# Kernel tuning notes

Hardware: AMD Instinct MI355X
Metric: run time of the kernel (lower is better)

Reference implementation:

```python
import jax, jax.numpy as jnp
import numpy as np

N_NODES = 100000
N_EDGES = 1600000
N_GRAPHS = 256
D = 128      # d_graph
H = 256      # hidden
VOCAB = 30000
OUT = 2


def setup_inputs() -> dict:
    key = jax.random.key(0)
    ks = jax.random.split(key, 24)
    def lin(k, fin, fout):
        s = 1.0 / np.sqrt(fin)
        kw, kb = jax.random.split(k)
        return (jax.random.uniform(kw, (fin, fout), jnp.float32, -s, s),
                jax.random.uniform(kb, (fout,), jnp.float32, -s, s))
    inp = {
        'feat': jax.random.randint(ks[0], (N_NODES,), 0, VOCAB),
        'src': jax.random.randint(ks[1], (N_EDGES,), 0, N_NODES),
        'dst': jax.random.randint(ks[2], (N_EDGES,), 0, N_NODES),
        'graph_id': jnp.sort(jax.random.randint(ks[3], (N_NODES,), 0, N_GRAPHS)),
        'emb': jax.random.normal(ks[4], (VOCAB, D), jnp.float32),
    }
    # SAGEConv layer 0/1: fc_self + fc_neigh + bias (mean aggregator)
    inp['ws0'], _ = lin(ks[5], D, D)
    inp['wn0'], inp['b0'] = lin(ks[6], D, D)
    inp['ws1'], _ = lin(ks[7], D, D)
    inp['wn1'], inp['b1'] = lin(ks[8], D, D)
    inp['e1_w'], inp['e1_b'] = lin(ks[9], D, H)
    inp['e2_w'], inp['e2_b'] = lin(ks[10], H, H)
    inp['e3_w'], inp['e3_b'] = lin(ks[11], H, H)
    inp['e4_w'], inp['e4_b'] = lin(ks[12], H, H)
    inp['pred_w'], inp['pred_b'] = lin(ks[13], H, OUT)
    return inp


def _sage_mean(h, src, dst, ws, wn, b):
    # gather src features, mean-scatter to dst (DGL SAGEConv 'mean')
    msg = jnp.take(h, src, axis=0)                       # [E, D]
    agg = jax.ops.segment_sum(msg, dst, num_segments=N_NODES)
    deg = jax.ops.segment_sum(jnp.ones((src.shape[0],), h.dtype), dst,
                              num_segments=N_NODES)
    h_neigh = agg / jnp.maximum(deg, 1.0)[:, None]
    return h @ ws + h_neigh @ wn + b


def reference(feat, src, dst, graph_id, emb,
              ws0, wn0, b0, ws1, wn1, b1,
              e1_w, e1_b, e2_w, e2_b, e3_w, e3_b, e4_w, e4_b,
              pred_w, pred_b):
    h = jnp.take(emb, feat, axis=0)                      # [N, D]
    h = jax.nn.relu(_sage_mean(h, src, dst, ws0, wn0, b0))
    h = jax.nn.relu(_sage_mean(h, src, dst, ws1, wn1, b1))
    # dgl.mean_nodes: per-graph mean pool
    gsum = jax.ops.segment_sum(h, graph_id, num_segments=N_GRAPHS)
    gcnt = jax.ops.segment_sum(jnp.ones((N_NODES,), h.dtype), graph_id,
                               num_segments=N_GRAPHS)
    hg = gsum / jnp.maximum(gcnt, 1.0)[:, None]          # [B, D]
    hidden = jax.nn.relu(hg @ e1_w + e1_b)
    h2 = jax.nn.relu(hidden @ e2_w + e2_b)
    h3 = jax.nn.relu(h2 @ e3_w + e3_b)
    h4 = jax.nn.relu(h3 @ e4_w + e4_b)
    y = h4 @ pred_w + pred_b
    return jax.nn.log_softmax(y, axis=1), hidden
```

## Files before the change

kernel.cpp:

```cpp
#include <hip/hip_runtime.h>
#include <hip/hip_bf16.h>
#include <math.h>

#define DF 128
#define HID 256
#define NG 256

typedef __attribute__((ext_vector_type(8))) short s8v;
typedef __attribute__((ext_vector_type(4))) float f32x4;
typedef __attribute__((ext_vector_type(2))) float f32x2;

__device__ __forceinline__ unsigned pack2bf(float lo, float hi){
  unsigned a = __bfloat16_as_ushort(__float2bfloat16(lo));
  unsigned b = __bfloat16_as_ushort(__float2bfloat16(hi));
  return a | (b<<16);
}

__global__ __launch_bounds__(256)
void k_pre(const int* __restrict__ feat, const float* __restrict__ emb,
           unsigned* __restrict__ h_f8,
           const int* __restrict__ dst, int* __restrict__ gb,
           const int* __restrict__ gid, float* __restrict__ gcnt,
           const float* __restrict__ ws0, const float* __restrict__ wn0,
           const float* __restrict__ ws1, const float* __restrict__ wn1,
           unsigned short* __restrict__ wt,
           int N, int E, int NE){
  __shared__ int hist[256];
  const int b = blockIdx.x, t = threadIdx.x;
  if (b < NE){
    int idx = b*256 + t;
    int total = N*(DF/8);
    if (idx<total){
      int i = idx/(DF/8), c = idx%(DF/8);
      const float4* e4 = (const float4*)emb;
      size_t rb = (size_t)feat[i]*(DF/4);
      float4 v0 = e4[rb + c*2], v1 = e4[rb + c*2+1];
      unsigned w0 = __builtin_amdgcn_cvt_pk_fp8_f32(v0.x, v0.y, 0, false);
      w0 = __builtin_amdgcn_cvt_pk_fp8_f32(v0.z, v0.w, w0, true);
      unsigned w1 = __builtin_amdgcn_cvt_pk_fp8_f32(v1.x, v1.y, 0, false);
      w1 = __builtin_amdgcn_cvt_pk_fp8_f32(v1.z, v1.w, w1, true);
      ((uint2*)h_f8)[idx] = make_uint2(w0,w1);
    }
  } else if (b < NE+256){
    int bb = b - NE;
    hist[t]=0; __syncthreads();
    for (int i = bb*256+t; i < E; i += 256*256)
      atomicAdd(&hist[dst[i]>>9], 1);
    __syncthreads();
    if (hist[t]) atomicAdd(&gb[t], hist[t]);
  } else if (b < NE+512){
    int bb = b - (NE+256);
    hist[t]=0; __syncthreads();
    for (int i = bb*256+t; i < N; i += 256*256)
      atomicAdd(&hist[gid[i]], 1);
    __syncthreads();
    if (hist[t]) atomicAdd(&gcnt[t], (float)hist[t]);
  } else {
    int bb = b - (NE+512);
    int n = bb & 127;
    int layer = bb >> 7;
    const float* ws = layer? ws1 : ws0;
    const float* wn = layer? wn1 : wn0;
    float v = (t<128)? ws[t*DF+n] : wn[(t-128)*DF+n];
    wt[((size_t)layer*DF + n)*256 + t] = __bfloat16_as_ushort(__float2bfloat16(v));
  }
}

__global__ void k_bscan(const int* __restrict__ gb, int* __restrict__ bbase,
                        int* __restrict__ bcur, int E){
  __shared__ int sh[256];
  int t = threadIdx.x;
  int v = gb[t];
  sh[t]=v; __syncthreads();
  for (int o=1;o<256;o<<=1){
    int x = (t>=o)? sh[t-o] : 0;
    __syncthreads();
    sh[t]+=x;
    __syncthreads();
  }
  int ex = sh[t]-v;
  bbase[t]=ex; bcur[t]=ex;
  if (t==255) bbase[256]=E;
}

__global__ __launch_bounds__(256)
void k_bplace(const int* __restrict__ src, const int* __restrict__ dst,
              int* __restrict__ bcur, unsigned* __restrict__ pairs, int E){
  __shared__ int hist[256];
  __shared__ int base[256];
  __shared__ int cur[256];
  const int t = threadIdx.x;
  const int CH = (E + gridDim.x - 1)/gridDim.x;
  const int s = blockIdx.x*CH;
  int e = s+CH; if (e>E) e=E;
  if (s>=E) return;
  hist[t]=0; __syncthreads();
  for (int i=s+t; i<e; i+=256) atomicAdd(&hist[dst[i]>>9],1);
  __syncthreads();
  if (hist[t]){ base[t]=atomicAdd(&bcur[t],hist[t]); }
  cur[t]=0;
  __syncthreads();
  for (int i=s+t; i<e; i+=256){
    int d = dst[i];
    int bk = d>>9;
    int r = atomicAdd(&cur[bk],1);
    pairs[base[bk]+r] = ((unsigned)src[i]<<9) | (unsigned)(d & 511);
  }
}

__global__ __launch_bounds__(256)
void k_bcsr(const unsigned* __restrict__ pairs, const int* __restrict__ bbase,
            int* __restrict__ offs, int* __restrict__ csr, int N, int E){
  __shared__ int ncnt[512];
  __shared__ int noff[512];
  __shared__ int sh[256];
  const int t = threadIdx.x;
  const int b = blockIdx.x;
  const int nb0 = b<<9;
  const int s = bbase[b], e = bbase[b+1];
  ncnt[t]=0; ncnt[t+256]=0;
  __syncthreads();
  for (int i=s+t; i<e; i+=256) atomicAdd(&ncnt[pairs[i] & 511u], 1);
  __syncthreads();
  int v0 = ncnt[2*t], v1 = ncnt[2*t+1];
  int v = v0+v1;
  sh[t]=v; __syncthreads();
  for (int o=1;o<256;o<<=1){
    int x=(t>=o)?sh[t-o]:0;
    __syncthreads();
    sh[t]+=x;
    __syncthreads();
  }
  int ex = sh[t]-v;
  noff[2*t]=ex; noff[2*t+1]=ex+v0;
  __syncthreads();
  {
    int n0 = nb0 + t;
    if (n0 < N) offs[n0] = s + noff[t];
    int n1 = nb0 + t + 256;
    if (n1 < N) offs[n1] = s + noff[t+256];
    if (b == gridDim.x-1 && t==0) offs[N] = E;
  }
  ncnt[t]=0; ncnt[t+256]=0;
  __syncthreads();
  for (int i=s+t; i<e; i+=256){
    unsigned p = pairs[i];
    int d = p & 511u;
    int r = atomicAdd(&ncnt[d],1);
    csr[s + noff[d] + r] = (int)(p >> 9);
  }
}

template<int MODE>
__global__ __launch_bounds__(256,6)
void k_sage(const unsigned char* __restrict__ h_in_f8,
            const int* __restrict__ offs, const int* __restrict__ csr,
            const unsigned short* __restrict__ wt,
            const float* __restrict__ bias,
            unsigned char* __restrict__ h_out_f8,
            const int* __restrict__ gid, float* __restrict__ gsum, int N){
  __shared__ __align__(16) unsigned short s_ab[32*256];
  __shared__ int s_gid[32];
  __shared__ float s_tmp[DF];
  const int t = threadIdx.x;
  const int node0 = blockIdx.x*32;
  const uint4* f8r = (const uint4*)h_in_f8;

  if (MODE==1 && t<32) s_gid[t] = (node0+t<N)? gid[node0+t] : -1;

  const int nn = t>>3, c = t&7;
  const int sw = (nn&7)<<4;

  {
    int node = node0+nn;
    uint4 q = make_uint4(0,0,0,0);
    if (node<N) q = f8r[(size_t)node*8 + c];
    f32x2 u; unsigned pk[8];
    u=__builtin_amdgcn_cvt_pk_f32_fp8(q.x,false); pk[0]=pack2bf(u[0],u[1]);
    u=__builtin_amdgcn_cvt_pk_f32_fp8(q.x,true ); pk[1]=pack2bf(u[0],u[1]);
    u=__builtin_amdgcn_cvt_pk_f32_fp8(q.y,false); pk[2]=pack2bf(u[0],u[1]);
    u=__builtin_amdgcn_cvt_pk_f32_fp8(q.y,true ); pk[3]=pack2bf(u[0],u[1]);
    u=__builtin_amdgcn_cvt_pk_f32_fp8(q.z,false); pk[4]=pack2bf(u[0],u[1]);
    u=__builtin_amdgcn_cvt_pk_f32_fp8(q.z,true ); pk[5]=pack2bf(u[0],u[1]);
    u=__builtin_amdgcn_cvt_pk_f32_fp8(q.w,false); pk[6]=pack2bf(u[0],u[1]);
    u=__builtin_amdgcn_cvt_pk_f32_fp8(q.w,true ); pk[7]=pack2bf(u[0],u[1]);
    int byte0 = nn*512 + c*32;
    *(uint4*)((char*)s_ab + ((byte0   )^sw)) = make_uint4(pk[0],pk[1],pk[2],pk[3]);
    *(uint4*)((char*)s_ab + ((byte0+16)^sw)) = make_uint4(pk[4],pk[5],pk[6],pk[7]);
  }

  {
    const int node = node0+nn;
    float a[16];
    #pragma unroll
    for (int j=0;j<16;j++) a[j]=0.f;
    if (node<N){
      int e0=offs[node], e1=offs[node+1];
      int deg = e1-e0;
      if (deg>0){
        #define ACC16(q) { \
          f32x2 u; \
          u=__builtin_amdgcn_cvt_pk_f32_fp8((q).x,false); a[0]+=u[0]; a[1]+=u[1]; \
          u=__builtin_amdgcn_cvt_pk_f32_fp8((q).x,true ); a[2]+=u[0]; a[3]+=u[1]; \
          u=__builtin_amdgcn_cvt_pk_f32_fp8((q).y,false); a[4]+=u[0]; a[5]+=u[1]; \
          u=__builtin_amdgcn_cvt_pk_f32_fp8((q).y,true ); a[6]+=u[0]; a[7]+=u[1]; \
          u=__builtin_amdgcn_cvt_pk_f32_fp8((q).z,false); a[8]+=u[0]; a[9]+=u[1]; \
          u=__builtin_amdgcn_cvt_pk_f32_fp8((q).z,true ); a[10]+=u[0]; a[11]+=u[1]; \
          u=__builtin_amdgcn_cvt_pk_f32_fp8((q).w,false); a[12]+=u[0]; a[13]+=u[1]; \
          u=__builtin_amdgcn_cvt_pk_f32_fp8((q).w,true ); a[14]+=u[0]; a[15]+=u[1]; }
        int e = e0;
        if (e & 1){
          uint4 q0 = f8r[(size_t)csr[e]*8 + c];
          ACC16(q0);
          e++;
        }
        for (; e+2<=e1; e+=2){
          int2 ss = *(const int2*)&csr[e];
          uint4 q0 = f8r[(size_t)ss.x*8 + c];
          uint4 q1 = f8r[(size_t)ss.y*8 + c];
          ACC16(q0); ACC16(q1);
        }
        if (e<e1){
          uint4 q0 = f8r[(size_t)csr[e]*8 + c];
          ACC16(q0);
        }
        #undef ACC16
        float inv = 1.0f/(float)deg;
        #pragma unroll
        for (int j=0;j<16;j++) a[j]*=inv;
      }
    }
    unsigned pk[8];
    #pragma unroll
    for (int j=0;j<8;j++) pk[j] = pack2bf(a[2*j],a[2*j+1]);
    int byte0 = nn*512 + 256 + c*32;
    *(uint4*)((char*)s_ab + ((byte0   )^sw)) = make_uint4(pk[0],pk[1],pk[2],pk[3]);
    *(uint4*)((char*)s_ab + ((byte0+16)^sw)) = make_uint4(pk[4],pk[5],pk[6],pk[7]);
  }

  const int wv = t>>6;
  const int lr = t&15;
  const int kg = (t&63)>>4;
  __syncthreads();

  f32x4 acc00={0,0,0,0}, acc01={0,0,0,0}, acc10={0,0,0,0}, acc11={0,0,0,0};
  const s8v* wt8 = (const s8v*)wt;
  #pragma unroll
  for (int kh=0; kh<2; kh++){
    s8v bfrag[2][4];
    #pragma unroll
    for (int ks=0; ks<4; ks++){
      int kb = (kh*4+ks)*4 + kg;
      bfrag[0][ks] = wt8[(size_t)(wv*32     + lr)*32 + kb];
      bfrag[1][ks] = wt8[(size_t)(wv*32 + 16+ lr)*32 + kb];
    }
    #pragma unroll
    for (int ks=0; ks<4; ks++){
      int cb = (kh*4+ks)*64 + kg*16;
      int r0 = lr, r1 = 16+lr;
      s8v a0 = *(const s8v*)((const char*)s_ab + ((r0*512+cb) ^ ((r0&7)<<4)));
      s8v a1 = *(const s8v*)((const char*)s_ab + ((r1*512+cb) ^ ((r1&7)<<4)));
      acc00 = __builtin_amdgcn_mfma_f32_16x16x32_bf16(a0, bfrag[0][ks], acc00, 0,0,0);
      acc01 = __builtin_amdgcn_mfma_f32_16x16x32_bf16(a0, bfrag[1][ks], acc01, 0,0,0);
      acc10 = __builtin_amdgcn_mfma_f32_16x16x32_bf16(a1, bfrag[0][ks], acc10, 0,0,0);
      acc11 = __builtin_amdgcn_mfma_f32_16x16x32_bf16(a1, bfrag[1][ks], acc11, 0,0,0);
    }
  }
  __syncthreads();

  float* cbuf = (float*)s_ab;
  #pragma unroll
  for (int r=0;r<4;r++){
    int row0 = kg*4 + r;
    cbuf[(row0   )*DF + wv*32      + lr] = acc00[r];
    cbuf[(row0   )*DF + wv*32 + 16 + lr] = acc01[r];
    cbuf[(row0+16)*DF + wv*32      + lr] = acc10[r];
    cbuf[(row0+16)*DF + wv*32 + 16 + lr] = acc11[r];
  }
  __syncthreads();

  if (MODE==0){
    int row = t>>3, c0 = (t&7)*16;
    int node = node0+row;
    if (node<N){
      float x[16];
      #pragma unroll
      for (int j=0;j<16;j++) x[j] = fmaxf(cbuf[row*DF + c0 + j] + bias[c0+j], 0.f);
      unsigned f0 = __builtin_amdgcn_cvt_pk_fp8_f32(x[0], x[1], 0, false);
      f0 = __builtin_amdgcn_cvt_pk_fp8_f32(x[2], x[3], f0, true);
      unsigned f1 = __builtin_amdgcn_cvt_pk_fp8_f32(x[4], x[5], 0, false);
      f1 = __builtin_amdgcn_cvt_pk_fp8_f32(x[6], x[7], f1, true);
      unsigned f2 = __builtin_amdgcn_cvt_pk_fp8_f32(x[8], x[9], 0, false);
      f2 = __builtin_amdgcn_cvt_pk_fp8_f32(x[10], x[11], f2, true);
      unsigned f3 = __builtin_amdgcn_cvt_pk_fp8_f32(x[12], x[13], 0, false);
      f3 = __builtin_amdgcn_cvt_pk_fp8_f32(x[14], x[15], f3, true);
      *(uint4*)&h_out_f8[(size_t)node*DF + c0] = make_uint4(f0,f1,f2,f3);
    }
  } else {
    const int d = t&127, rh = t>>7;
    const float bd = bias[d];
    int segStart = 0;
    while (segStart < 32 && s_gid[segStart] >= 0){
      int g = s_gid[segStart];
      int segEnd = segStart+1;
      while (segEnd < 32 && s_gid[segEnd] == g) segEnd++;
      float p = 0.f;
      for (int r = segStart+rh; r < segEnd; r += 2)
        p += fmaxf(cbuf[r*DF + d] + bd, 0.f);
      if (rh==1) s_tmp[d] = p;
      __syncthreads();
      if (rh==0) atomicAdd(&gsum[g*DF+d], p + s_tmp[d]);
      __syncthreads();
      segStart = segEnd;
    }
  }
}

__global__ __launch_bounds__(256)
void k_head(const float* __restrict__ gsum, const float* __restrict__ gcnt,
            const float* __restrict__ e1w, const float* __restrict__ e1b,
            const float* __restrict__ e2w, const float* __restrict__ e2b,
            const float* __restrict__ e3w, const float* __restrict__ e3b,
            const float* __restrict__ e4w, const float* __restrict__ e4b,
            const float* __restrict__ pw,  const float* __restrict__ pb,
            float* __restrict__ out, float* __restrict__ hidden){
  __shared__ float hg[DF];
  __shared__ float bufA[HID];
  __shared__ float bufB[HID];
  __shared__ float r0[HID], r1[HID];
  const int g = blockIdx.x, t = threadIdx.x;
  if (t<DF) hg[t] = gsum[g*DF+t] / fmaxf(gcnt[g],1.0f);
  __syncthreads();

  float acc = e1b[t];
  for (int k=0;k<DF;++k) acc += hg[k]*e1w[k*HID+t];
  float h1 = fmaxf(acc,0.f);
  hidden[g*HID+t] = h1;
  bufA[t] = h1;
  __syncthreads();

  acc = e2b[t];
  for (int k=0;k<HID;++k) acc += bufA[k]*e2w[k*HID+t];
  bufB[t] = fmaxf(acc,0.f);
  __syncthreads();

  acc = e3b[t];
  for (int k=0;k<HID;++k) acc += bufB[k]*e3w[k*HID+t];
  bufA[t] = fmaxf(acc,0.f);
  __syncthreads();

  acc = e4b[t];
  for (int k=0;k<HID;++k) acc += bufA[k]*e4w[k*HID+t];
  float h4 = fmaxf(acc,0.f);

  r0[t] = h4*pw[t*2+0];
  r1[t] = h4*pw[t*2+1];
  __syncthreads();
  for (int o=128;o>0;o>>=1){
    if (t<o){ r0[t]+=r0[t+o]; r1[t]+=r1[t+o]; }
    __syncthreads();
  }
  if (t==0){
    float y0 = r0[0]+pb[0], y1 = r1[0]+pb[1];
    float m = fmaxf(y0,y1);
    float l = m + logf(expf(y0-m)+expf(y1-m));
    out[g*2+0]=y0-l;
    out[g*2+1]=y1-l;
  }
}

extern "C" void kernel_launch(void* const* d_in, const int* in_sizes, int n_in,
                              void* d_out, int out_size, void* d_ws, size_t ws_size,
                              hipStream_t stream){
  const int* feat = (const int*)d_in[0];
  const int* src  = (const int*)d_in[1];
  const int* dst  = (const int*)d_in[2];
  const int* gid  = (const int*)d_in[3];
  const float* emb = (const float*)d_in[4];
  const float* ws0 = (const float*)d_in[5];
  const float* wn0 = (const float*)d_in[6];
  const float* b0  = (const float*)d_in[7];
  const float* ws1 = (const float*)d_in[8];
  const float* wn1 = (const float*)d_in[9];
  const float* b1  = (const float*)d_in[10];
  const float* e1w = (const float*)d_in[11];
  const float* e1b = (const float*)d_in[12];
  const float* e2w = (const float*)d_in[13];
  const float* e2b = (const float*)d_in[14];
  const float* e3w = (const float*)d_in[15];
  const float* e3b = (const float*)d_in[16];
  const float* e4w = (const float*)d_in[17];
  const float* e4b = (const float*)d_in[18];
  const float* pw  = (const float*)d_in[19];
  const float* pb  = (const float*)d_in[20];
  const int N = in_sizes[0];
  const int E = in_sizes[1];

  char* basep = (char*)d_ws;
  size_t off=0;
  auto alloc=[&](size_t bytes)->void*{
    void* p = basep+off; off=(off+bytes+255)&~(size_t)255; return p;
  };
  unsigned char*  hA_f8 = (unsigned char*) alloc((size_t)N*DF);
  unsigned char*  hB_f8 = (unsigned char*) alloc((size_t)N*DF);
  int*   offs  = (int*)  alloc((size_t)(N+1)*4);
  int*   csr   = (int*)  alloc((size_t)E*4);
  int*   gb    = (int*)  alloc(1024);
  int*   bbase = (int*)  alloc(1056);
  int*   bcur  = (int*)  alloc(1024);
  unsigned short* wtb = (unsigned short*)alloc((size_t)2*DF*256*2);
  float* gsum  = (float*)alloc((size_t)NG*DF*4);
  float* gcnt  = (float*)alloc((size_t)NG*4);
  unsigned* pairs = (unsigned*)alloc((size_t)E*4);
  float* out    = (float*)d_out;
  float* hidden = out + NG*2;

  hipMemsetAsync(gb, 0, 1024, stream);
  hipMemsetAsync(gsum, 0, (size_t)NG*DF*4, stream);
  hipMemsetAsync(gcnt, 0, (size_t)NG*4, stream);

  const int NBK = (N+511)>>9;
  const int NE = (N*(DF/8) + 255)/256;
  k_pre<<<NE+768,256,0,stream>>>(feat,emb,(unsigned*)hA_f8,
                                 dst,gb,gid,gcnt,
                                 ws0,wn0,ws1,wn1,wtb,N,E,NE);
  k_bscan<<<1,256,0,stream>>>(gb,bbase,bcur,E);
  k_bplace<<<256,256,0,stream>>>(src,dst,bcur,pairs,E);
  k_bcsr<<<NBK,256,0,stream>>>(pairs,bbase,offs,csr,N,E);

  k_sage<0><<<(N+31)/32,256,0,stream>>>(hA_f8,offs,csr,wtb,        b0,
                                        hB_f8,nullptr,nullptr,N);
  k_sage<1><<<(N+31)/32,256,0,stream>>>(hB_f8,offs,csr,wtb+DF*256, b1,
                                        nullptr,gid,gsum,N);

  k_head<<<NG,HID,0,stream>>>(gsum,gcnt,e1w,e1b,e2w,e2b,e3w,e3b,e4w,e4b,
                              pw,pb,out,hidden);
}
```

Baseline: 219.7 us.

## Convert embedding table to fp8 once, fold bucket scan into consumers, raise occupancy

The whole 30000-row embedding table is now converted to fp8 in one pass. A separate kernel then gathers fp8 rows per node, replacing the per-node fp32 gather and conversion. The standalone single-block bucket scan kernel is removed, and each k_bplace and k_bcsr block redundantly rescans the 256 bucket counts in shared memory. A memset of bcur is added in its place. The k_sage launch bounds go from 6 to 8 blocks per SM, which trades register budget for occupancy.

```diff
diff --git a/kernel.cpp b/kernel.cpp
--- a/kernel.cpp
+++ b/kernel.cpp
@@ -17,46 +17,43 @@
 }
 
 __global__ __launch_bounds__(256)
-void k_pre(const int* __restrict__ feat, const float* __restrict__ emb,
-           unsigned* __restrict__ h_f8,
-           const int* __restrict__ dst, int* __restrict__ gb,
-           const int* __restrict__ gid, float* __restrict__ gcnt,
-           const float* __restrict__ ws0, const float* __restrict__ wn0,
-           const float* __restrict__ ws1, const float* __restrict__ wn1,
-           unsigned short* __restrict__ wt,
-           int N, int E, int NE){
+void k_pre0(const float* __restrict__ emb, unsigned* __restrict__ emb_f8, int nvoc,
+            const int* __restrict__ dst, int* __restrict__ gb,
+            const int* __restrict__ gid, float* __restrict__ gcnt,
+            const float* __restrict__ ws0, const float* __restrict__ wn0,
+            const float* __restrict__ ws1, const float* __restrict__ wn1,
+            unsigned short* __restrict__ wt,
+            int N, int E, int NC){
   __shared__ int hist[256];
   const int b = blockIdx.x, t = threadIdx.x;
-  if (b < NE){
+  if (b < NC){
     int idx = b*256 + t;
-    int total = N*(DF/8);
+    int total = nvoc*(DF/8);
     if (idx<total){
-      int i = idx/(DF/8), c = idx%(DF/8);
       const float4* e4 = (const float4*)emb;
-      size_t rb = (size_t)feat[i]*(DF/4);
-      float4 v0 = e4[rb + c*2], v1 = e4[rb + c*2+1];
+      float4 v0 = e4[(size_t)idx*2], v1 = e4[(size_t)idx*2+1];
       unsigned w0 = __builtin_amdgcn_cvt_pk_fp8_f32(v0.x, v0.y, 0, false);
       w0 = __builtin_amdgcn_cvt_pk_fp8_f32(v0.z, v0.w, w0, true);
       unsigned w1 = __builtin_amdgcn_cvt_pk_fp8_f32(v1.x, v1.y, 0, false);
       w1 = __builtin_amdgcn_cvt_pk_fp8_f32(v1.z, v1.w, w1, true);
-      ((uint2*)h_f8)[idx] = make_uint2(w0,w1);
-    }
-  } else if (b < NE+256){
-    int bb = b - NE;
+      ((uint2*)emb_f8)[idx] = make_uint2(w0,w1);
+    }
+  } else if (b < NC+256){
+    int bb = b - NC;
     hist[t]=0; __syncthreads();
     for (int i = bb*256+t; i < E; i += 256*256)
       atomicAdd(&hist[dst[i]>>9], 1);
     __syncthreads();
     if (hist[t]) atomicAdd(&gb[t], hist[t]);
-  } else if (b < NE+512){
-    int bb = b - (NE+256);
+  } else if (b < NC+512){
+    int bb = b - (NC+256);
     hist[t]=0; __syncthreads();
     for (int i = bb*256+t; i < N; i += 256*256)
       atomicAdd(&hist[gid[i]], 1);
     __syncthreads();
     if (hist[t]) atomicAdd(&gcnt[t], (float)hist[t]);
   } else {
-    int bb = b - (NE+512);
+    int bb = b - (NC+512);
     int n = bb & 127;
     int layer = bb >> 7;
     const float* ws = layer? ws1 : ws0;
@@ -66,26 +63,22 @@
   }
 }
 
-__global__ void k_bscan(const int* __restrict__ gb, int* __restrict__ bbase,
-                        int* __restrict__ bcur, int E){
-  __shared__ int sh[256];
-  int t = threadIdx.x;
-  int v = gb[t];
-  sh[t]=v; __syncthreads();
-  for (int o=1;o<256;o<<=1){
-    int x = (t>=o)? sh[t-o] : 0;
-    __syncthreads();
-    sh[t]+=x;
-    __syncthreads();
-  }
-  int ex = sh[t]-v;
-  bbase[t]=ex; bcur[t]=ex;
-  if (t==255) bbase[256]=E;
+__global__ __launch_bounds__(256)
+void k_pre1(const int* __restrict__ feat, const unsigned* __restrict__ emb_f8,
+            unsigned* __restrict__ h_f8, int N){
+  int idx = blockIdx.x*256 + threadIdx.x;
+  int total = N*8;
+  if (idx<total){
+    int i = idx>>3, c = idx&7;
+    ((uint4*)h_f8)[idx] = ((const uint4*)emb_f8)[(size_t)feat[i]*8 + c];
+  }
 }
 
 __global__ __launch_bounds__(256)
 void k_bplace(const int* __restrict__ src, const int* __restrict__ dst,
-              int* __restrict__ bcur, unsigned* __restrict__ pairs, int E){
+              const int* __restrict__ gb, int* __restrict__ bcur,
+              unsigned* __restrict__ pairs, int E){
+  __shared__ int sgb[256];
   __shared__ int hist[256];
   __shared__ int base[256];
   __shared__ int cur[256];
@@ -94,10 +87,20 @@
   const int s = blockIdx.x*CH;
   int e = s+CH; if (e>E) e=E;
   if (s>=E) return;
-  hist[t]=0; __syncthreads();
+  int v = gb[t];
+  sgb[t]=v;
+  hist[t]=0;
+  __syncthreads();
+  for (int o=1;o<256;o<<=1){
+    int x = (t>=o)? sgb[t-o] : 0;
+    __syncthreads();
+    sgb[t]+=x;
+    __syncthreads();
+  }
+  int bstart = sgb[t]-v;
   for (int i=s+t; i<e; i+=256) atomicAdd(&hist[dst[i]>>9],1);
   __syncthreads();
-  if (hist[t]){ base[t]=atomicAdd(&bcur[t],hist[t]); }
+  if (hist[t]){ base[t] = bstart + atomicAdd(&bcur[t],hist[t]); }
   cur[t]=0;
   __syncthreads();
   for (int i=s+t; i<e; i+=256){
@@ -109,29 +112,39 @@
 }
 
 __global__ __launch_bounds__(256)
-void k_bcsr(const unsigned* __restrict__ pairs, const int* __restrict__ bbase,
+void k_bcsr(const unsigned* __restrict__ pairs, const int* __restrict__ gb,
             int* __restrict__ offs, int* __restrict__ csr, int N, int E){
+  __shared__ int sgb[256];
   __shared__ int ncnt[512];
   __shared__ int noff[512];
   __shared__ int sh[256];
   const int t = threadIdx.x;
   const int b = blockIdx.x;
   const int nb0 = b<<9;
-  const int s = bbase[b], e = bbase[b+1];
+  int v = gb[t];
+  sgb[t]=v;
   ncnt[t]=0; ncnt[t+256]=0;
   __syncthreads();
+  for (int o=1;o<256;o<<=1){
+    int x = (t>=o)? sgb[t-o] : 0;
+    __syncthreads();
+    sgb[t]+=x;
+    __syncthreads();
+  }
+  const int s = sgb[b]-gb[b];
+  const int e = sgb[b];
   for (int i=s+t; i<e; i+=256) atomicAdd(&ncnt[pairs[i] & 511u], 1);
   __syncthreads();
   int v0 = ncnt[2*t], v1 = ncnt[2*t+1];
-  int v = v0+v1;
-  sh[t]=v; __syncthreads();
+  int vv = v0+v1;
+  sh[t]=vv; __syncthreads();
   for (int o=1;o<256;o<<=1){
     int x=(t>=o)?sh[t-o]:0;
     __syncthreads();
     sh[t]+=x;
     __syncthreads();
   }
-  int ex = sh[t]-v;
+  int ex = sh[t]-vv;
   noff[2*t]=ex; noff[2*t+1]=ex+v0;
   __syncthreads();
   {
@@ -152,7 +165,7 @@
 }
 
 template<int MODE>
-__global__ __launch_bounds__(256,6)
+__global__ __launch_bounds__(256,8)
 void k_sage(const unsigned char* __restrict__ h_in_f8,
             const int* __restrict__ offs, const int* __restrict__ csr,
             const unsigned short* __restrict__ wt,
@@ -395,6 +408,7 @@
   const float* pb  = (const float*)d_in[20];
   const int N = in_sizes[0];
   const int E = in_sizes[1];
+  const int nvoc = in_sizes[4] / DF;
 
   char* basep = (char*)d_ws;
   size_t off=0;
@@ -403,10 +417,10 @@
   };
   unsigned char*  hA_f8 = (unsigned char*) alloc((size_t)N*DF);
   unsigned char*  hB_f8 = (unsigned char*) alloc((size_t)N*DF);
+  unsigned char*  emb_f8= (unsigned char*) alloc((size_t)nvoc*DF);
   int*   offs  = (int*)  alloc((size_t)(N+1)*4);
   int*   csr   = (int*)  alloc((size_t)E*4);
   int*   gb    = (int*)  alloc(1024);
-  int*   bbase = (int*)  alloc(1056);
   int*   bcur  = (int*)  alloc(1024);
   unsigned short* wtb = (unsigned short*)alloc((size_t)2*DF*256*2);
   float* gsum  = (float*)alloc((size_t)NG*DF*4);
@@ -416,17 +430,19 @@
   float* hidden = out + NG*2;
 
   hipMemsetAsync(gb, 0, 1024, stream);
+  hipMemsetAsync(bcur, 0, 1024, stream);
   hipMemsetAsync(gsum, 0, (size_t)NG*DF*4, stream);
   hipMemsetAsync(gcnt, 0, (size_t)NG*4, stream);
 
   const int NBK = (N+511)>>9;
-  const int NE = (N*(DF/8) + 255)/256;
-  k_pre<<<NE+768,256,0,stream>>>(feat,emb,(unsigned*)hA_f8,
-                                 dst,gb,gid,gcnt,
-                                 ws0,wn0,ws1,wn1,wtb,N,E,NE);
-  k_bscan<<<1,256,0,stream>>>(gb,bbase,bcur,E);
-  k_bplace<<<256,256,0,stream>>>(src,dst,bcur,pairs,E);
-  k_bcsr<<<NBK,256,0,stream>>>(pairs,bbase,offs,csr,N,E);
+  const int NC = (nvoc*(DF/8) + 255)/256;
+  k_pre0<<<NC+768,256,0,stream>>>(emb,(unsigned*)emb_f8,nvoc,
+                                  dst,gb,gid,gcnt,
+                                  ws0,wn0,ws1,wn1,wtb,N,E,NC);
+  k_pre1<<<(N*8+255)/256,256,0,stream>>>(feat,(const unsigned*)emb_f8,
+                                         (unsigned*)hA_f8,N);
+  k_bplace<<<256,256,0,stream>>>(src,dst,gb,bcur,pairs,E);
+  k_bcsr<<<NBK,256,0,stream>>>(pairs,gb,offs,csr,N,E);
 
   k_sage<0><<<(N+31)/32,256,0,stream>>>(hA_f8,offs,csr,wtb,        b0,
                                         hB_f8,nullptr,nullptr,N);
```

New measurement: 220.8 us. Within noise of the previous version (+0.5%).
